# Performance work log

Hardware: AMD Instinct MI355X
Metric: run time of the kernel (lower is better)

Reference implementation:

```python
import jax, jax.numpy as jnp
import numpy as np

EPS = 1e-5

def _bn(h, g, b, m, v):
    # h: (B, Ch, L); BatchNorm1d in eval mode over channel axis 1
    inv = jax.lax.rsqrt(v + EPS)
    return (h - m[None, :, None]) * (inv * g)[None, :, None] + b[None, :, None]

def setup_inputs() -> dict:
    key = jax.random.key(0)
    ks = jax.random.split(key, 12)
    B, C, N = 32, 256, 4096
    N8, C8 = N // 8, C // 8
    x = jax.random.normal(ks[0], (B, C, N), dtype=jnp.float32)
    Wq = jax.random.normal(ks[1], (N8, N), dtype=jnp.float32) * (1.0 / np.sqrt(N))
    Wk = jax.random.normal(ks[2], (N8, N), dtype=jnp.float32) * (1.0 / np.sqrt(N))
    bn1_g = jnp.ones((N8,), jnp.float32); bn1_b = jnp.zeros((N8,), jnp.float32)
    bn1_m = jax.random.normal(ks[3], (N8,), jnp.float32) * 0.1
    bn1_v = jax.random.uniform(ks[4], (N8,), jnp.float32, 0.5, 1.5)
    bn2_g = jnp.ones((N8,), jnp.float32); bn2_b = jnp.zeros((N8,), jnp.float32)
    bn2_m = jax.random.normal(ks[5], (N8,), jnp.float32) * 0.1
    bn2_v = jax.random.uniform(ks[6], (N8,), jnp.float32, 0.5, 1.5)
    W1 = jax.random.normal(ks[7], (C8, C), dtype=jnp.float32) * (1.0 / np.sqrt(C))
    W2 = jax.random.normal(ks[8], (C, C8), dtype=jnp.float32) * (1.0 / np.sqrt(C8))
    alpha = jax.random.normal(ks[9], (1,), dtype=jnp.float32)
    return {"x": x, "Wq": Wq, "bn1_g": bn1_g, "bn1_b": bn1_b, "bn1_m": bn1_m, "bn1_v": bn1_v,
            "Wk": Wk, "bn2_g": bn2_g, "bn2_b": bn2_b, "bn2_m": bn2_m, "bn2_v": bn2_v,
            "W1": W1, "W2": W2, "alpha": alpha}

def reference(x, Wq, bn1_g, bn1_b, bn1_m, bn1_v, Wk, bn2_g, bn2_b, bn2_m, bn2_v, W1, W2, alpha):
    # x: (B, C, N); x_hat: (B, N, C) -- conv1d with kernel 1 == matmul over N axis
    x_hat = jnp.transpose(x, (0, 2, 1))
    q = jax.nn.relu(_bn(jnp.einsum('qn,bnc->bqc', Wq, x_hat), bn1_g, bn1_b, bn1_m, bn1_v))  # (B, N8, C)
    k = jax.nn.relu(_bn(jnp.einsum('qn,bnc->bqc', Wk, x_hat), bn2_g, bn2_b, bn2_m, bn2_v))  # (B, N8, C)
    sim = jnp.einsum('bkc,bkd->bcd', k, q)  # (B, C, C)
    aff = jax.nn.softmax(jnp.max(sim, axis=-1, keepdims=True) - sim, axis=-1)
    # squeeze-excite gating over channels
    pooled = jnp.max(x, axis=-1)  # (B, C) AdaptiveMaxPool1d(1)
    s = jax.nn.sigmoid(jax.nn.relu(pooled @ W1.T) @ W2.T)  # (B, C)
    gated = x * s[:, :, None]
    out = alpha[0] * jnp.einsum('bcd,bdn->bcn', aff, gated) + x
    return out
```

## Files before the change

kernel.cpp:

```cpp
#include <hip/hip_runtime.h>
#include <math.h>

#define B_   32
#define C_   256
#define N_   4096
#define N8_  512
#define C8_  32
#define EPS_ 1e-5f

typedef __attribute__((ext_vector_type(8))) short short8;
typedef __attribute__((ext_vector_type(4))) float f32x4;

__device__ __forceinline__ ushort f2bf(float v) {
  unsigned u = __float_as_uint(v);
  unsigned r = (u + 0x7fffu + ((u >> 16) & 1u)) >> 16;
  return (ushort)r;
}
__device__ __forceinline__ float bf2f(ushort h) {
  return __uint_as_float(((unsigned)h) << 16);
}

__global__ __launch_bounds__(256) void k_cvt(const float* __restrict__ src,
                                             ushort* __restrict__ hi,
                                             ushort* __restrict__ lo, int n4) {
  int i = blockIdx.x * 256 + threadIdx.x;
  int stride = gridDim.x * 256;
  for (; i < n4; i += stride) {
    float4 v = ((const float4*)src)[i];
    ushort4 h, l;
    h.x = f2bf(v.x); l.x = f2bf(v.x - bf2f(h.x));
    h.y = f2bf(v.y); l.y = f2bf(v.y - bf2f(h.y));
    h.z = f2bf(v.z); l.z = f2bf(v.z - bf2f(h.z));
    h.w = f2bf(v.w); l.w = f2bf(v.w - bf2f(h.w));
    ((ushort4*)hi)[i] = h;
    ((ushort4*)lo)[i] = l;
  }
}

__global__ __launch_bounds__(256) void k_cvt_x(const float* __restrict__ x,
    ushort* __restrict__ xh, ushort* __restrict__ xl,
    ushort* __restrict__ xTh, float* __restrict__ partial) {
  int b = blockIdx.z, cb = blockIdx.y, nb = blockIdx.x;
  int t = threadIdx.x;
  int cl  = t >> 2;
  int nl0 = (t & 3) * 16;
  const float* xp = x + ((size_t)b * C_ + cb * 64 + cl) * N_ + nb * 64 + nl0;
  float v[16];
  *(float4*)&v[0]  = *(const float4*)(xp + 0);
  *(float4*)&v[4]  = *(const float4*)(xp + 4);
  *(float4*)&v[8]  = *(const float4*)(xp + 8);
  *(float4*)&v[12] = *(const float4*)(xp + 12);
  ushort h[16], l[16];
  float mx = -3.402823466e+38f;
  #pragma unroll
  for (int j = 0; j < 16; ++j) {
    h[j] = f2bf(v[j]);
    l[j] = f2bf(v[j] - bf2f(h[j]));
    mx = fmaxf(mx, v[j]);
  }
  size_t fbase = ((size_t)b * C_ + cb * 64 + cl) * N_ + nb * 64 + nl0;
  *(short8*)(xh + fbase)     = *(short8*)&h[0];
  *(short8*)(xh + fbase + 8) = *(short8*)&h[8];
  *(short8*)(xl + fbase)     = *(short8*)&l[0];
  *(short8*)(xl + fbase + 8) = *(short8*)&l[8];
  mx = fmaxf(mx, __shfl_xor(mx, 1, 64));
  mx = fmaxf(mx, __shfl_xor(mx, 2, 64));
  if ((t & 3) == 0)
    partial[((size_t)b * C_ + cb * 64 + cl) * 64 + nb] = mx;
  __shared__ ushort lds[64 * 66];
  #pragma unroll
  for (int j = 0; j < 16; ++j) lds[cl * 66 + nl0 + j] = h[j];
  __syncthreads();
  int nr = t >> 2;
  int c0 = (t & 3) * 16;
  ushort o[16];
  #pragma unroll
  for (int j = 0; j < 16; ++j) o[j] = lds[(c0 + j) * 66 + nr];
  size_t tbase = ((size_t)b * N_ + nb * 64 + nr) * C_ + cb * 64 + c0;
  *(short8*)(xTh + tbase)     = *(short8*)&o[0];
  *(short8*)(xTh + tbase + 8) = *(short8*)&o[8];
}

__global__ __launch_bounds__(256) void k_semlp(const float* __restrict__ partial,
                                               const float* __restrict__ W1,
                                               const float* __restrict__ W2,
                                               float* __restrict__ s) {
  int b = blockIdx.x, t = threadIdx.x;
  __shared__ float p[C_];
  __shared__ float h[C8_];
  float m = -3.402823466e+38f;
  const float* pp = partial + ((size_t)b * C_ + t) * 64;
  #pragma unroll
  for (int j = 0; j < 64; ++j) m = fmaxf(m, pp[j]);
  p[t] = m;
  __syncthreads();
  if (t < C8_) {
    float a = 0.f;
    for (int c = 0; c < C_; ++c) a = fmaf(p[c], W1[t * C_ + c], a);
    h[t] = fmaxf(a, 0.f);
  }
  __syncthreads();
  float a = 0.f;
  #pragma unroll
  for (int j = 0; j < C8_; ++j) a = fmaf(h[j], W2[t * C8_ + j], a);
  s[b * C_ + t] = 1.f / (1.f + __expf(-a));
}

__global__ __launch_bounds__(256) void k_qk_mfma(
    const ushort* __restrict__ Wh, const ushort* __restrict__ Wl,
    const ushort* __restrict__ Xh, const ushort* __restrict__ Xl,
    const float* __restrict__ g1, const float* __restrict__ b1,
    const float* __restrict__ m1, const float* __restrict__ v1,
    const float* __restrict__ g2, const float* __restrict__ b2,
    const float* __restrict__ m2, const float* __restrict__ v2,
    float* __restrict__ q, float* __restrict__ k) {
  int b  = blockIdx.z;
  int rb = blockIdx.y;
  int cb = blockIdx.x;
  __shared__ ushort Ah[128 * 32];
  __shared__ ushort Al[128 * 32];
  __shared__ ushort Bh[128 * 32];
  __shared__ ushort Bl[128 * 32];
  int t = threadIdx.x, wave = t >> 6, lane = t & 63;
  int wr = (wave >> 1) * 64, wc = (wave & 1) * 64;
  int srow = wave * 16 + (lane >> 2);
  int skof = (lane & 3) * 8;
  size_t aoff = (size_t)(rb * 128 + srow) * N_ + skof;
  size_t boff = ((size_t)b * C_ + cb * 128 + srow) * N_ + skof;
  int lb0 = (wave * 16) * 32;

  f32x4 acc[4][4];
  #pragma unroll
  for (int mi = 0; mi < 4; ++mi)
    #pragma unroll
    for (int ni = 0; ni < 4; ++ni)
      acc[mi][ni] = (f32x4){0.f, 0.f, 0.f, 0.f};

  int fr = lane & 15, quad = lane >> 4;
  for (int k0 = 0; k0 < N_; k0 += 32) {
    #pragma unroll
    for (int seg = 0; seg < 2; ++seg) {
      size_t ga = aoff + (size_t)seg * 64 * N_ + k0;
      size_t gb = boff + (size_t)seg * 64 * N_ + k0;
      int lb = lb0 + seg * 64 * 32;
      __builtin_amdgcn_global_load_lds(
          (const __attribute__((address_space(1))) void*)(Wh + ga),
          (__attribute__((address_space(3))) void*)(&Ah[lb]), 16, 0, 0);
      __builtin_amdgcn_global_load_lds(
          (const __attribute__((address_space(1))) void*)(Wl + ga),
          (__attribute__((address_space(3))) void*)(&Al[lb]), 16, 0, 0);
      __builtin_amdgcn_global_load_lds(
          (const __attribute__((address_space(1))) void*)(Xh + gb),
          (__attribute__((address_space(3))) void*)(&Bh[lb]), 16, 0, 0);
      __builtin_amdgcn_global_load_lds(
          (const __attribute__((address_space(1))) void*)(Xl + gb),
          (__attribute__((address_space(3))) void*)(&Bl[lb]), 16, 0, 0);
    }
    __syncthreads();
    short8 af[4][2], bf[4][2];
    #pragma unroll
    for (int i = 0; i < 4; ++i) {
      int ra = (wr + i * 16 + fr) * 32 + quad * 8;
      af[i][0] = *(const short8*)&Ah[ra];
      af[i][1] = *(const short8*)&Al[ra];
      int rbx = (wc + i * 16 + fr) * 32 + quad * 8;
      bf[i][0] = *(const short8*)&Bh[rbx];
      bf[i][1] = *(const short8*)&Bl[rbx];
    }
    #pragma unroll
    for (int mi = 0; mi < 4; ++mi)
      #pragma unroll
      for (int ni = 0; ni < 4; ++ni) {
        acc[mi][ni] = __builtin_amdgcn_mfma_f32_16x16x32_bf16(
            af[mi][0], bf[ni][0], acc[mi][ni], 0, 0, 0);
        acc[mi][ni] = __builtin_amdgcn_mfma_f32_16x16x32_bf16(
            af[mi][0], bf[ni][1], acc[mi][ni], 0, 0, 0);
        acc[mi][ni] = __builtin_amdgcn_mfma_f32_16x16x32_bf16(
            af[mi][1], bf[ni][0], acc[mi][ni], 0, 0, 0);
      }
    __syncthreads();
  }

  bool isq = rb < 4;
  const float* G  = isq ? g1 : g2;
  const float* Bp = isq ? b1 : b2;
  const float* Mn = isq ? m1 : m2;
  const float* Vv = isq ? v1 : v2;
  float* dst = (isq ? q : k) + (size_t)b * N8_ * C_;
  int mrow0 = (isq ? rb : rb - 4) * 128 + wr + quad * 4;
  int cgl = cb * 128 + wc + fr;
  #pragma unroll
  for (int mi = 0; mi < 4; ++mi) {
    #pragma unroll
    for (int r = 0; r < 4; ++r) {
      int m = mrow0 + mi * 16 + r;
      float sc = G[m] * rsqrtf(Vv[m] + EPS_);
      float bi = Bp[m] - Mn[m] * sc;
      #pragma unroll
      for (int ni = 0; ni < 4; ++ni) {
        float v = fmaxf(fmaf(acc[mi][ni][r], sc, bi), 0.f);
        dst[(size_t)m * C_ + cgl + ni * 16] = v;
      }
    }
  }
}

__global__ __launch_bounds__(256) void k_simsoft(const float* __restrict__ q,
    const float* __restrict__ k, const float* __restrict__ s,
    const float* __restrict__ alpha, ushort* __restrict__ aff2) {
  int b = blockIdx.y, ct = blockIdx.x;
  int t = threadIdx.x;
  __shared__ float kT[N8_][16];
  const float* kb = k + (size_t)b * N8_ * C_;
  int c0 = ct * 16;
  for (int chunk = 0; chunk < N8_ / 16; ++chunk) {
    int row = chunk * 16 + (t >> 4);
    kT[row][t & 15] = kb[(size_t)row * C_ + c0 + (t & 15)];
  }
  __syncthreads();
  float acc[16];
  #pragma unroll
  for (int i = 0; i < 16; ++i) acc[i] = 0.f;
  const float* qb = q + (size_t)b * N8_ * C_;
  for (int kk = 0; kk < N8_; ++kk) {
    float qv = qb[(size_t)kk * C_ + t];
    float4 k0 = *(const float4*)&kT[kk][0];
    float4 k1 = *(const float4*)&kT[kk][4];
    float4 k2 = *(const float4*)&kT[kk][8];
    float4 k3 = *(const float4*)&kT[kk][12];
    acc[0]  = fmaf(k0.x, qv, acc[0]);  acc[1]  = fmaf(k0.y, qv, acc[1]);
    acc[2]  = fmaf(k0.z, qv, acc[2]);  acc[3]  = fmaf(k0.w, qv, acc[3]);
    acc[4]  = fmaf(k1.x, qv, acc[4]);  acc[5]  = fmaf(k1.y, qv, acc[5]);
    acc[6]  = fmaf(k1.z, qv, acc[6]);  acc[7]  = fmaf(k1.w, qv, acc[7]);
    acc[8]  = fmaf(k2.x, qv, acc[8]);  acc[9]  = fmaf(k2.y, qv, acc[9]);
    acc[10] = fmaf(k2.z, qv, acc[10]); acc[11] = fmaf(k2.w, qv, acc[11]);
    acc[12] = fmaf(k3.x, qv, acc[12]); acc[13] = fmaf(k3.y, qv, acc[13]);
    acc[14] = fmaf(k3.z, qv, acc[14]); acc[15] = fmaf(k3.w, qv, acc[15]);
  }
  int lane = t & 63, wid = t >> 6;
  __shared__ float wmin[16][4];
  __shared__ float wsum[16][4];
  #pragma unroll
  for (int i = 0; i < 16; ++i) {
    float v = acc[i];
    for (int off = 32; off > 0; off >>= 1) v = fminf(v, __shfl_xor(v, off, 64));
    if (lane == 0) wmin[i][wid] = v;
  }
  __syncthreads();
  float w[16];
  #pragma unroll
  for (int i = 0; i < 16; ++i) {
    float m = fminf(fminf(wmin[i][0], wmin[i][1]), fminf(wmin[i][2], wmin[i][3]));
    w[i] = __expf(m - acc[i]);
  }
  #pragma unroll
  for (int i = 0; i < 16; ++i) {
    float v = w[i];
    for (int off = 32; off > 0; off >>= 1) v += __shfl_xor(v, off, 64);
    if (lane == 0) wsum[i][wid] = v;
  }
  __syncthreads();
  float fac = alpha[0] * s[b * C_ + t];
  ushort* ab = aff2 + (size_t)b * C_ * C_;
  #pragma unroll
  for (int i = 0; i < 16; ++i) {
    float Z = wsum[i][0] + wsum[i][1] + wsum[i][2] + wsum[i][3];
    ab[(size_t)(c0 + i) * C_ + t] = f2bf(fac * w[i] / Z);
  }
}

__global__ __launch_bounds__(256) void k_out_mfma(
    const ushort* __restrict__ aff, const ushort* __restrict__ xTh,
    const float* __restrict__ x, float* __restrict__ out) {
  int b  = blockIdx.z;
  int cb = blockIdx.y;
  int nb = blockIdx.x;
  __shared__ ushort Ah[128 * 32];
  __shared__ ushort Bh[128 * 32];
  int t = threadIdx.x, wave = t >> 6, lane = t & 63;
  int wr = (wave >> 1) * 64, wc = (wave & 1) * 64;
  int srow = wave * 16 + (lane >> 2);
  int skof = (lane & 3) * 8;
  size_t aoff = ((size_t)b * C_ + cb * 128 + srow) * C_ + skof;
  size_t boff = ((size_t)b * N_ + nb * 128 + srow) * C_ + skof;
  int lb0 = (wave * 16) * 32;

  f32x4 acc[4][4];
  #pragma unroll
  for (int mi = 0; mi < 4; ++mi)
    #pragma unroll
    for (int ni = 0; ni < 4; ++ni)
      acc[mi][ni] = (f32x4){0.f, 0.f, 0.f, 0.f};

  int fr = lane & 15, quad = lane >> 4;
  for (int k0 = 0; k0 < C_; k0 += 32) {
    #pragma unroll
    for (int seg = 0; seg < 2; ++seg) {
      size_t ga = aoff + (size_t)seg * 64 * C_ + k0;
      size_t gb = boff + (size_t)seg * 64 * C_ + k0;
      int lb = lb0 + seg * 64 * 32;
      __builtin_amdgcn_global_load_lds(
          (const __attribute__((address_space(1))) void*)(aff + ga),
          (__attribute__((address_space(3))) void*)(&Ah[lb]), 16, 0, 0);
      __builtin_amdgcn_global_load_lds(
          (const __attribute__((address_space(1))) void*)(xTh + gb),
          (__attribute__((address_space(3))) void*)(&Bh[lb]), 16, 0, 0);
    }
    __syncthreads();
    short8 af[4], bf[4];
    #pragma unroll
    for (int i = 0; i < 4; ++i) {
      af[i] = *(const short8*)&Ah[(wr + i * 16 + fr) * 32 + quad * 8];
      bf[i] = *(const short8*)&Bh[(wc + i * 16 + fr) * 32 + quad * 8];
    }
    #pragma unroll
    for (int mi = 0; mi < 4; ++mi)
      #pragma unroll
      for (int ni = 0; ni < 4; ++ni)
        acc[mi][ni] = __builtin_amdgcn_mfma_f32_16x16x32_bf16(
            af[mi], bf[ni], acc[mi][ni], 0, 0, 0);
    __syncthreads();
  }

  const float* xb = x + (size_t)b * C_ * N_;
  float* ob = out + (size_t)b * C_ * N_;
  int c0 = cb * 128 + wr + quad * 4;
  int n0 = nb * 128 + wc + fr;
  #pragma unroll
  for (int mi = 0; mi < 4; ++mi) {
    #pragma unroll
    for (int r = 0; r < 4; ++r) {
      int c = c0 + mi * 16 + r;
      #pragma unroll
      for (int ni = 0; ni < 4; ++ni) {
        int n = n0 + ni * 16;
        ob[(size_t)c * N_ + n] = acc[mi][ni][r] + xb[(size_t)c * N_ + n];
      }
    }
  }
}

extern "C" void kernel_launch(void* const* d_in, const int* in_sizes, int n_in,
                              void* d_out, int out_size, void* d_ws, size_t ws_size,
                              hipStream_t stream) {
  const float* x     = (const float*)d_in[0];
  const float* Wq    = (const float*)d_in[1];
  const float* g1    = (const float*)d_in[2];
  const float* b1    = (const float*)d_in[3];
  const float* m1    = (const float*)d_in[4];
  const float* v1    = (const float*)d_in[5];
  const float* Wk    = (const float*)d_in[6];
  const float* g2    = (const float*)d_in[7];
  const float* b2    = (const float*)d_in[8];
  const float* m2    = (const float*)d_in[9];
  const float* v2    = (const float*)d_in[10];
  const float* W1    = (const float*)d_in[11];
  const float* W2    = (const float*)d_in[12];
  const float* alpha = (const float*)d_in[13];
  float* out = (float*)d_out;

  float* ws      = (float*)d_ws;
  float* q       = ws;
  float* kbuf    = q + (size_t)B_ * N8_ * C_;
  float* partial = kbuf + (size_t)B_ * N8_ * C_;
  float* s       = partial + (size_t)B_ * C_ * 64;
  ushort* aff    = (ushort*)(s + B_ * C_);
  ushort* xh     = aff + (size_t)B_ * C_ * C_;
  ushort* xl     = xh + (size_t)B_ * C_ * N_;
  ushort* xTh    = xl + (size_t)B_ * C_ * N_;
  ushort* wh     = xTh + (size_t)B_ * C_ * N_;
  ushort* wl     = wh + (size_t)2 * N8_ * N_;

  k_cvt_x<<<dim3(64, 4, B_), 256, 0, stream>>>(x, xh, xl, xTh, partial);
  k_cvt<<<dim3(1024), 256, 0, stream>>>(Wq, wh, wl, N8_ * N_ / 4);
  k_cvt<<<dim3(1024), 256, 0, stream>>>(Wk, wh + (size_t)N8_ * N_,
                                        wl + (size_t)N8_ * N_, N8_ * N_ / 4);
  k_semlp<<<dim3(B_), 256, 0, stream>>>(partial, W1, W2, s);
  k_qk_mfma<<<dim3(2, 8, B_), 256, 0, stream>>>(wh, wl, xh, xl,
                                                g1, b1, m1, v1,
                                                g2, b2, m2, v2, q, kbuf);
  k_simsoft<<<dim3(16, B_), 256, 0, stream>>>(q, kbuf, s, alpha, aff);
  k_out_mfma<<<dim3(32, 2, B_), 256, 0, stream>>>(aff, xTh, x, out);
}
```

Before: 682.9 us.

## Rewrite QK projection GEMM with 256x256 tiles, split-K, and software pipelining

Replaces the 128x128 bf16-split QK GEMM with a 512-thread kernel using 256x256 tiles, XOR-swizzled LDS, double-buffered global-to-LDS loads interleaved with MFMA issue, and s_setprio. The three hi/lo product terms are flattened into a 192-step K loop that is split across two blocks. The split-K partials go to the output buffer as scratch, and a new reduction kernel adds them and applies BatchNorm and ReLU. This aims to raise MFMA utilization and overlap memory with compute, at the cost of an extra partial-sum write and read and an extra launch.

```diff
diff --git a/kernel.cpp b/kernel.cpp
--- a/kernel.cpp
+++ b/kernel.cpp
@@ -106,103 +106,178 @@
   s[b * C_ + t] = 1.f / (1.f + __expf(-a));
 }
 
-__global__ __launch_bounds__(256) void k_qk_mfma(
-    const ushort* __restrict__ Wh, const ushort* __restrict__ Wl,
-    const ushort* __restrict__ Xh, const ushort* __restrict__ Xl,
+#define GLD16(SRC, DSTP) __builtin_amdgcn_global_load_lds( \
+    (const __attribute__((address_space(1))) void*)(SRC), \
+    (__attribute__((address_space(3))) void*)(DSTP), 16, 0, 0)
+
+__global__ __launch_bounds__(512, 2) void k_qk8(
+    const ushort* __restrict__ wh, const ushort* __restrict__ wl,
+    const ushort* __restrict__ xh, const ushort* __restrict__ xl,
+    float* __restrict__ part) {
+  __shared__ ushort lds[2][2][256 * 64];
+  const int ks = blockIdx.x;
+  const int mt = blockIdx.y;
+  const int b  = blockIdx.z;
+  const int t = threadIdx.x;
+  const int lane = t & 63, wave = t >> 6;
+  const int wm = wave >> 2, wn = wave & 3;
+  const int fr = lane & 15, quad = lane >> 4;
+  const int R0 = mt * 256;
+  const int tr = t >> 3, tc = (t & 7) << 3;
+  int aro[4], bro[4];
+#pragma unroll
+  for (int j = 0; j < 4; ++j) {
+    int rl = j * 64 + tr;
+    int cu = tc ^ (((rl >> 2) & 1) << 4);
+    aro[j] = (R0 + rl) * N_ + cu;
+    bro[j] = (b * C_ + rl) * N_ + cu;
+  }
+  const int dl = t * 8;
+
+  f32x4 acc[8][4];
+#pragma unroll
+  for (int m = 0; m < 8; ++m)
+#pragma unroll
+    for (int n = 0; n < 4; ++n) acc[m][n] = (f32x4){0.f, 0.f, 0.f, 0.f};
+
+  short8 af[4][2];
+  short8 bf[2][2][2];
+
+#define STG_A(AP, K0, P, J0) do { \
+    GLD16((AP) + (aro[J0] + (K0)), &lds[P][0][(J0) * 4096 + dl]); \
+    GLD16((AP) + (aro[(J0) + 1] + (K0)), &lds[P][0][((J0) + 1) * 4096 + dl]); \
+  } while (0)
+#define STG_B(BP, K0, P, J0) do { \
+    GLD16((BP) + (bro[J0] + (K0)), &lds[P][1][(J0) * 4096 + dl]); \
+    GLD16((BP) + (bro[(J0) + 1] + (K0)), &lds[P][1][((J0) + 1) * 4096 + dl]); \
+  } while (0)
+#define VMC(N) asm volatile("s_waitcnt vmcnt(" #N ")" ::: "memory")
+#define BARF() do { __builtin_amdgcn_s_barrier(); \
+                    __builtin_amdgcn_sched_barrier(0); } while (0)
+#define RDA(P, MH) do { \
+    _Pragma("unroll") \
+    for (int m = 0; m < 4; ++m) { \
+      int r = wm * 128 + ((MH) * 4 + m) * 16 + fr; \
+      int o = (r << 6) + (quad << 3); \
+      int fx = ((r >> 2) & 1) << 4; \
+      af[m][0] = *(const short8*)&lds[P][0][o ^ fx]; \
+      af[m][1] = *(const short8*)&lds[P][0][(o + 32) ^ fx]; \
+    } } while (0)
+#define RDB(P, NH) do { \
+    _Pragma("unroll") \
+    for (int n = 0; n < 2; ++n) { \
+      int c = wn * 64 + ((NH) * 2 + n) * 16 + fr; \
+      int o = (c << 6) + (quad << 3); \
+      int fx = ((c >> 2) & 1) << 4; \
+      bf[NH][n][0] = *(const short8*)&lds[P][1][o ^ fx]; \
+      bf[NH][n][1] = *(const short8*)&lds[P][1][(o + 32) ^ fx]; \
+    } } while (0)
+#define MMQ(MH, NH) do { \
+    __builtin_amdgcn_s_setprio(1); \
+    _Pragma("unroll") \
+    for (int m = 0; m < 4; ++m) \
+      _Pragma("unroll") \
+      for (int n = 0; n < 2; ++n) { \
+        acc[(MH)*4+m][(NH)*2+n] = __builtin_amdgcn_mfma_f32_16x16x32_bf16( \
+            af[m][0], bf[NH][n][0], acc[(MH)*4+m][(NH)*2+n], 0, 0, 0); \
+        acc[(MH)*4+m][(NH)*2+n] = __builtin_amdgcn_mfma_f32_16x16x32_bf16( \
+            af[m][1], bf[NH][n][1], acc[(MH)*4+m][(NH)*2+n], 0, 0, 0); \
+      } \
+    __builtin_amdgcn_s_setprio(0); } while (0)
+
+  const int gbase = ks * 96;
+  {
+    int g = gbase, sg = g >> 6, k0 = (g & 63) << 6;
+    const ushort* Ap = (sg == 1) ? wl : wh;
+    const ushort* Bp = (sg == 2) ? xl : xh;
+    STG_A(Ap, k0, 0, 0); STG_A(Ap, k0, 0, 2);
+    STG_B(Bp, k0, 0, 0); STG_B(Bp, k0, 0, 2);
+    int g1 = gbase + 1, s1 = g1 >> 6, k1 = (g1 & 63) << 6;
+    const ushort* Ap1 = (s1 == 1) ? wl : wh;
+    STG_A(Ap1, k1, 1, 0);
+  }
+
+#pragma unroll 1
+  for (int i = 0; i < 48; ++i) {
+    int gO = gbase + 2 * i + 1, sO = gO >> 6, kO = (gO & 63) << 6;
+    const ushort* AO = (sO == 1) ? wl : wh;
+    const ushort* BO = (sO == 2) ? xl : xh;
+    int gE = gbase + 2 * i + 2, sE = gE >> 6, kE = (gE & 63) << 6;
+    const ushort* AE = (sE == 1) ? wl : wh;
+    const ushort* BE = (sE == 2) ? xl : xh;
+    int gP = gbase + 2 * i + 3, sP = gP >> 6, kP = (gP & 63) << 6;
+    const ushort* APn = (sP == 1) ? wl : wh;
+    const bool nl = (i < 47);
+    STG_A(AO, kO, 1, 2);
+    VMC(4); BARF();
+    RDA(0, 0); RDB(0, 0); MMQ(0, 0);
+    STG_B(BO, kO, 1, 0);
+    RDB(0, 1); MMQ(0, 1);
+    STG_B(BO, kO, 1, 2);
+    RDA(0, 1); MMQ(1, 0);
+    BARF();
+    if (nl) STG_A(AE, kE, 0, 0);
+    MMQ(1, 1);
+    if (nl) { STG_A(AE, kE, 0, 2); VMC(4); } else { VMC(0); }
+    BARF();
+    RDA(1, 0); RDB(1, 0); MMQ(0, 0);
+    if (nl) STG_B(BE, kE, 0, 0);
+    RDB(1, 1); MMQ(0, 1);
+    if (nl) STG_B(BE, kE, 0, 2);
+    RDA(1, 1); MMQ(1, 0);
+    BARF();
+    if (nl) STG_A(APn, kP, 1, 0);
+    MMQ(1, 1);
+  }
+
+  float* dst = part + ((size_t)(ks * 32 + b) * 1024) * 256;
+#pragma unroll
+  for (int m = 0; m < 8; ++m) {
+    int row0 = R0 + wm * 128 + m * 16 + quad * 4;
+#pragma unroll
+    for (int r = 0; r < 4; ++r) {
+#pragma unroll
+      for (int n = 0; n < 4; ++n) {
+        int col = wn * 64 + n * 16 + fr;
+        dst[(size_t)(row0 + r) * 256 + col] = acc[m][n][r];
+      }
+    }
+  }
+#undef STG_A
+#undef STG_B
+#undef VMC
+#undef BARF
+#undef RDA
+#undef RDB
+#undef MMQ
+}
+
+__global__ __launch_bounds__(256) void k_qkred(
+    const float* __restrict__ part,
     const float* __restrict__ g1, const float* __restrict__ b1,
     const float* __restrict__ m1, const float* __restrict__ v1,
     const float* __restrict__ g2, const float* __restrict__ b2,
     const float* __restrict__ m2, const float* __restrict__ v2,
     float* __restrict__ q, float* __restrict__ k) {
-  int b  = blockIdx.z;
-  int rb = blockIdx.y;
-  int cb = blockIdx.x;
-  __shared__ ushort Ah[128 * 32];
-  __shared__ ushort Al[128 * 32];
-  __shared__ ushort Bh[128 * 32];
-  __shared__ ushort Bl[128 * 32];
-  int t = threadIdx.x, wave = t >> 6, lane = t & 63;
-  int wr = (wave >> 1) * 64, wc = (wave & 1) * 64;
-  int srow = wave * 16 + (lane >> 2);
-  int skof = (lane & 3) * 8;
-  size_t aoff = (size_t)(rb * 128 + srow) * N_ + skof;
-  size_t boff = ((size_t)b * C_ + cb * 128 + srow) * N_ + skof;
-  int lb0 = (wave * 16) * 32;
-
-  f32x4 acc[4][4];
-  #pragma unroll
-  for (int mi = 0; mi < 4; ++mi)
-    #pragma unroll
-    for (int ni = 0; ni < 4; ++ni)
-      acc[mi][ni] = (f32x4){0.f, 0.f, 0.f, 0.f};
-
-  int fr = lane & 15, quad = lane >> 4;
-  for (int k0 = 0; k0 < N_; k0 += 32) {
-    #pragma unroll
-    for (int seg = 0; seg < 2; ++seg) {
-      size_t ga = aoff + (size_t)seg * 64 * N_ + k0;
-      size_t gb = boff + (size_t)seg * 64 * N_ + k0;
-      int lb = lb0 + seg * 64 * 32;
-      __builtin_amdgcn_global_load_lds(
-          (const __attribute__((address_space(1))) void*)(Wh + ga),
-          (__attribute__((address_space(3))) void*)(&Ah[lb]), 16, 0, 0);
-      __builtin_amdgcn_global_load_lds(
-          (const __attribute__((address_space(1))) void*)(Wl + ga),
-          (__attribute__((address_space(3))) void*)(&Al[lb]), 16, 0, 0);
-      __builtin_amdgcn_global_load_lds(
-          (const __attribute__((address_space(1))) void*)(Xh + gb),
-          (__attribute__((address_space(3))) void*)(&Bh[lb]), 16, 0, 0);
-      __builtin_amdgcn_global_load_lds(
-          (const __attribute__((address_space(1))) void*)(Xl + gb),
-          (__attribute__((address_space(3))) void*)(&Bl[lb]), 16, 0, 0);
-    }
-    __syncthreads();
-    short8 af[4][2], bf[4][2];
-    #pragma unroll
-    for (int i = 0; i < 4; ++i) {
-      int ra = (wr + i * 16 + fr) * 32 + quad * 8;
-      af[i][0] = *(const short8*)&Ah[ra];
-      af[i][1] = *(const short8*)&Al[ra];
-      int rbx = (wc + i * 16 + fr) * 32 + quad * 8;
-      bf[i][0] = *(const short8*)&Bh[rbx];
-      bf[i][1] = *(const short8*)&Bl[rbx];
-    }
-    #pragma unroll
-    for (int mi = 0; mi < 4; ++mi)
-      #pragma unroll
-      for (int ni = 0; ni < 4; ++ni) {
-        acc[mi][ni] = __builtin_amdgcn_mfma_f32_16x16x32_bf16(
-            af[mi][0], bf[ni][0], acc[mi][ni], 0, 0, 0);
-        acc[mi][ni] = __builtin_amdgcn_mfma_f32_16x16x32_bf16(
-            af[mi][0], bf[ni][1], acc[mi][ni], 0, 0, 0);
-        acc[mi][ni] = __builtin_amdgcn_mfma_f32_16x16x32_bf16(
-            af[mi][1], bf[ni][0], acc[mi][ni], 0, 0, 0);
-      }
-    __syncthreads();
-  }
-
-  bool isq = rb < 4;
-  const float* G  = isq ? g1 : g2;
-  const float* Bp = isq ? b1 : b2;
-  const float* Mn = isq ? m1 : m2;
-  const float* Vv = isq ? v1 : v2;
-  float* dst = (isq ? q : k) + (size_t)b * N8_ * C_;
-  int mrow0 = (isq ? rb : rb - 4) * 128 + wr + quad * 4;
-  int cgl = cb * 128 + wc + fr;
-  #pragma unroll
-  for (int mi = 0; mi < 4; ++mi) {
-    #pragma unroll
-    for (int r = 0; r < 4; ++r) {
-      int m = mrow0 + mi * 16 + r;
-      float sc = G[m] * rsqrtf(Vv[m] + EPS_);
-      float bi = Bp[m] - Mn[m] * sc;
-      #pragma unroll
-      for (int ni = 0; ni < 4; ++ni) {
-        float v = fmaxf(fmaf(acc[mi][ni][r], sc, bi), 0.f);
-        dst[(size_t)m * C_ + cgl + ni * 16] = v;
-      }
-    }
-  }
+  int i = blockIdx.x * 256 + threadIdx.x;
+  int b = i >> 16;
+  int rem = i & 65535;
+  int row = rem >> 6;
+  int c4 = (rem & 63) << 2;
+  const float4* p = (const float4*)part;
+  float4 u = p[i];
+  float4 w = p[i + 2097152];
+  bool isq = row < 512;
+  int m = isq ? row : row - 512;
+  float sc = (isq ? g1 : g2)[m] * rsqrtf((isq ? v1 : v2)[m] + EPS_);
+  float bi = (isq ? b1 : b2)[m] - (isq ? m1 : m2)[m] * sc;
+  float4 o;
+  o.x = fmaxf(fmaf(u.x + w.x, sc, bi), 0.f);
+  o.y = fmaxf(fmaf(u.y + w.y, sc, bi), 0.f);
+  o.z = fmaxf(fmaf(u.z + w.z, sc, bi), 0.f);
+  o.w = fmaxf(fmaf(u.w + w.w, sc, bi), 0.f);
+  float* d = (isq ? q : k) + ((size_t)b * N8_ + m) * C_ + c4;
+  *(float4*)d = o;
 }
 
 __global__ __launch_bounds__(256) void k_simsoft(const float* __restrict__ q,
@@ -371,14 +446,16 @@
   ushort* wh     = xTh + (size_t)B_ * C_ * N_;
   ushort* wl     = wh + (size_t)2 * N8_ * N_;
 
+  float* gpart = (float*)d_out;
+
   k_cvt_x<<<dim3(64, 4, B_), 256, 0, stream>>>(x, xh, xl, xTh, partial);
   k_cvt<<<dim3(1024), 256, 0, stream>>>(Wq, wh, wl, N8_ * N_ / 4);
   k_cvt<<<dim3(1024), 256, 0, stream>>>(Wk, wh + (size_t)N8_ * N_,
                                         wl + (size_t)N8_ * N_, N8_ * N_ / 4);
   k_semlp<<<dim3(B_), 256, 0, stream>>>(partial, W1, W2, s);
-  k_qk_mfma<<<dim3(2, 8, B_), 256, 0, stream>>>(wh, wl, xh, xl,
-                                                g1, b1, m1, v1,
-                                                g2, b2, m2, v2, q, kbuf);
+  k_qk8<<<dim3(2, 4, B_), 512, 0, stream>>>(wh, wl, xh, xl, gpart);
+  k_qkred<<<dim3(8192), 256, 0, stream>>>(gpart, g1, b1, m1, v1,
+                                          g2, b2, m2, v2, q, kbuf);
   k_simsoft<<<dim3(16, B_), 256, 0, stream>>>(q, kbuf, s, alpha, aff);
   k_out_mfma<<<dim3(32, 2, B_), 256, 0, stream>>>(aff, xTh, x, out);
 }
```

Result: faster. 663.9 us (-2.8%).
